# Optimization experiments

Hardware: AMD Instinct MI355X
Metric: run time of the kernel (lower is better)

The kernel has to match this reference:

```python
import jax, jax.numpy as jnp
import numpy as np

N, E, G = 200000, 800000, 8000
NODE_IN, EDGE_IN, H = 256, 64, 256


def _mlp2(h, w1, b1, w2, b2):
    return jax.nn.relu(h @ w1 + b1) @ w2 + b2


def setup_inputs() -> dict:
    key = jax.random.key(0)
    ks = jax.random.split(key, 30)
    s = 0.05
    p = lambda k, shp: (jax.random.normal(k, shp, jnp.float32) * s)
    inp = {
        "x": jax.random.normal(ks[0], (N, NODE_IN), jnp.float32),
        "edge_attr": jax.random.normal(ks[1], (E, EDGE_IN), jnp.float32),
        "edge_index": jax.random.randint(ks[2], (2, E), 0, N, dtype=jnp.int32),
        "batch": jnp.sort(jax.random.randint(ks[3], (N,), 0, G, dtype=jnp.int32)),
        # edge MLP
        "em_w1": p(ks[4], (EDGE_IN, H)), "em_b1": jnp.zeros((H,), jnp.float32),
        "em_w2": p(ks[5], (H, H)), "em_b2": jnp.zeros((H,), jnp.float32),
        # GINEConv 1 MLP
        "c1_w1": p(ks[6], (NODE_IN, H)), "c1_b1": jnp.zeros((H,), jnp.float32),
        "c1_w2": p(ks[7], (H, H)), "c1_b2": jnp.zeros((H,), jnp.float32),
        # GINEConv 2 MLP
        "c2_w1": p(ks[8], (H, H)), "c2_b1": jnp.zeros((H,), jnp.float32),
        "c2_w2": p(ks[9], (H, H)), "c2_b2": jnp.zeros((H,), jnp.float32),
        # heads
        "l1_w": p(ks[10], (H, 128)), "l1_b": jnp.zeros((128,), jnp.float32),
        "l2_w": p(ks[11], (128, 64)), "l2_b": jnp.zeros((64,), jnp.float32),
        "hS_w": p(ks[12], (64, 1)), "hS_b": jnp.zeros((1,), jnp.float32),
        "hP_w": p(ks[13], (64, 1)), "hP_b": jnp.zeros((1,), jnp.float32),
        "hN_w": p(ks[14], (64, 1)), "hN_b": jnp.zeros((1,), jnp.float32),
    }
    return inp


def _gine(x, ea, src, dst, w1, b1, w2, b2):
    # GINEConv (eps=0): out = MLP(x_i + sum_j relu(x_j + e_ji))
    msg = jax.nn.relu(x[src] + ea)                      # [E, H]
    agg = jax.ops.segment_sum(msg, dst, num_segments=x.shape[0])
    return _mlp2(x + agg, w1, b1, w2, b2)


def reference(x, edge_attr, edge_index, batch,
              em_w1, em_b1, em_w2, em_b2,
              c1_w1, c1_b1, c1_w2, c1_b2,
              c2_w1, c2_b1, c2_w2, c2_b2,
              l1_w, l1_b, l2_w, l2_b,
              hS_w, hS_b, hP_w, hP_b, hN_w, hN_b):
    src, dst = edge_index[0], edge_index[1]  # source_to_target flow
    ea = _mlp2(edge_attr, em_w1, em_b1, em_w2, em_b2)   # [E, 256]
    h = jax.nn.relu(_gine(x, ea, src, dst, c1_w1, c1_b1, c1_w2, c1_b2))
    h = jax.nn.relu(_gine(h, ea, src, dst, c2_w1, c2_b1, c2_w2, c2_b2))
    # global mean pool over graphs (dropout is identity in eval mode)
    sums = jax.ops.segment_sum(h, batch, num_segments=G)              # [G, 256]
    cnts = jax.ops.segment_sum(jnp.ones((h.shape[0],), h.dtype), batch, num_segments=G)
    pooled = sums / jnp.maximum(cnts, 1.0)[:, None]
    g = jax.nn.relu(pooled @ l1_w + l1_b)
    g = jax.nn.relu(g @ l2_w + l2_b)
    return ((g @ hS_w + hS_b).squeeze(-1),
            (g @ hP_w + hP_b).squeeze(-1),
            (g @ hN_w + hN_b).squeeze(-1))
```

## Files before the change

### kernel.cpp

```cpp
#include <hip/hip_runtime.h>
#include <hip/hip_bf16.h>

typedef __attribute__((ext_vector_type(8))) short short8;
typedef __attribute__((ext_vector_type(4))) float f32x4;
typedef __attribute__((ext_vector_type(2))) unsigned int u32x2;
typedef __attribute__((ext_vector_type(4))) unsigned int u32x4;

#define N_NODES  200000
#define N_EDGES  800000
#define N_GRAPHS 8000

__device__ __forceinline__ unsigned short f2bf(float f) {
  unsigned int u = __float_as_uint(f);
  unsigned int r = (u + 0x7fffu + ((u >> 16) & 1u)) >> 16;
  return (unsigned short)r;
}
__device__ __forceinline__ float bf2f(unsigned short s) {
  return __uint_as_float(((unsigned int)s) << 16);
}
__device__ __forceinline__ unsigned cvtpk(float a, float b) {
  union { __hip_bfloat162 h; unsigned u; } cv;
  cv.h = __float22bfloat162_rn(make_float2(a, b));
  return cv.u;
}

__device__ __forceinline__ void xpose4(unsigned W0, unsigned W1, int bsub,
                                       unsigned selT, unsigned& T0, unsigned& T1) {
  unsigned t0 = (unsigned)__shfl_xor((int)W0, 2);
  unsigned t1 = (unsigned)__shfl_xor((int)W1, 2);
  unsigned A0 = (bsub & 2) ? t1 : W0;
  unsigned A1 = (bsub & 2) ? W1 : t0;
  unsigned t2 = (unsigned)__shfl_xor((int)A0, 1);
  unsigned t3 = (unsigned)__shfl_xor((int)A1, 1);
  T0 = __builtin_amdgcn_perm(A0, t2, selT);
  T1 = __builtin_amdgcn_perm(A1, t3, selT);
}

__global__ void wtrans(const float* __restrict__ w, unsigned short* __restrict__ wt,
                       int K, int Nc) {
  int id = blockIdx.x * 256 + threadIdx.x;
  if (id >= K * Nc) return;
  int k = id / Nc, n = id % Nc;
  wt[n * K + k] = f2bf(w[id]);
}

__global__ __launch_bounds__(256) void f2bf_bulk(const float* __restrict__ x,
                                                 unsigned short* __restrict__ xb,
                                                 int n8) {
  int id = blockIdx.x * 256 + threadIdx.x;
  if (id >= n8) return;
  float4 a = ((const float4*)x)[id * 2];
  float4 b = ((const float4*)x)[id * 2 + 1];
  u32x4 pk = {cvtpk(a.x, a.y), cvtpk(a.z, a.w), cvtpk(b.x, b.y), cvtpk(b.z, b.w)};
  ((u32x4*)xb)[id] = pk;
}

template <int K1, int IN_MODE, int SLAB, int NKK>
__device__ __forceinline__ void stage_slab(
    int s, char* ab, int row0, int srow, int skk,
    const unsigned short* __restrict__ Xb,
    const unsigned short* __restrict__ aggb) {
#pragma unroll
  for (int c2 = 0; c2 < NKK; ++c2) {
    const int kloc = skk + 32 * c2;
    const int gk = s * SLAB + kloc;
    int off = srow * (2 * SLAB) + kloc * 2;
    off ^= (srow & 7) << 4;
    if (IN_MODE == 3) {
      u32x4 d = *(const u32x4*)(Xb + (size_t)(row0 + srow) * K1 + gk);
      *(u32x4*)(ab + off) = d;
    } else {
      const unsigned short* hp = Xb + (size_t)(row0 + srow) * 256 + gk;
      short8 hv = *(const short8*)hp;
      const unsigned short* ap = aggb + (size_t)(row0 + srow) * 256 + gk;
      short8 av = *(const short8*)ap;
      float v[8];
#pragma unroll
      for (int i = 0; i < 8; ++i)
        v[i] = bf2f((unsigned short)hv[i]) + bf2f((unsigned short)av[i]);
      u32x4 pk;
#pragma unroll
      for (int i = 0; i < 4; ++i) pk[i] = cvtpk(v[2 * i], v[2 * i + 1]);
      *(u32x4*)(ab + off) = pk;
    }
  }
}

template <int K1, int IN_MODE>
__global__ __launch_bounds__(256) void fused_mlp2(
    const unsigned short* __restrict__ Xb,
    const unsigned short* __restrict__ aggb,
    const unsigned short* __restrict__ w1t, const float* __restrict__ b1,
    const unsigned short* __restrict__ w2t, const float* __restrict__ b2,
    unsigned short* __restrict__ out, const int* __restrict__ perm,
    int relu_out) {
  constexpr int SLAB  = (K1 < 128) ? K1 : 128;
  constexpr int NSLAB = K1 / SLAB;
  constexpr int NKK   = SLAB / 32;
  __shared__ unsigned short h_lds[64 * 256];
  char* hbase = (char*)h_lds;

  const int tid  = threadIdx.x;
  const int row0 = blockIdx.x * 64;
  const int lane = tid & 63;
  const int wid  = tid >> 6;
  const int lr   = lane & 15;
  const int kq   = lane >> 4;
  const int col0 = wid * 64;
  const int bsub = lr & 3;
  const int asub = lr >> 2;
  const unsigned selT = (bsub & 1) ? 0x07060302u : 0x01000504u;

  const int srow = tid >> 2;
  const int skk  = (tid & 3) * 8;

  f32x4 acc[4][4];
#pragma unroll
  for (int m = 0; m < 4; ++m)
#pragma unroll
    for (int n = 0; n < 4; ++n) acc[m][n] = (f32x4){0.f, 0.f, 0.f, 0.f};

  float bias1[4];
#pragma unroll
  for (int n = 0; n < 4; ++n) bias1[n] = b1[col0 + n * 16 + lr];

  stage_slab<K1, IN_MODE, SLAB, NKK>(0, hbase, row0, srow, skk, Xb, aggb);
  __syncthreads();

#pragma unroll
  for (int s = 0; s < NSLAB; ++s) {
    if (s + 1 < NSLAB)
      stage_slab<K1, IN_MODE, SLAB, NKK>(s + 1, hbase + 16384, row0, srow, skk,
                                         Xb, aggb);
    char* ab = hbase + (s & 1) * 16384;
#pragma unroll
    for (int kk = 0; kk < NKK; ++kk) {
      short8 af[4], bq[4];
#pragma unroll
      for (int m = 0; m < 4; ++m) {
        int r = m * 16 + lr;
        int off = r * (2 * SLAB) + kk * 64 + kq * 16;
        off ^= (r & 7) << 4;
        af[m] = *(short8*)(ab + off);
      }
#pragma unroll
      for (int n = 0; n < 4; ++n) {
        int c = col0 + n * 16 + lr;
        bq[n] = *(const short8*)(w1t + (size_t)c * K1 + s * SLAB + kk * 32 + kq * 8);
      }
#pragma unroll
      for (int m = 0; m < 4; ++m)
#pragma unroll
        for (int n = 0; n < 4; ++n)
          acc[m][n] = __builtin_amdgcn_mfma_f32_16x16x32_bf16(af[m], bq[n], acc[m][n], 0, 0, 0);
    }
    __syncthreads();
  }

#pragma unroll
  for (int n = 0; n < 4; ++n) {
    float bn = bias1[n];
#pragma unroll
    for (int m = 0; m < 4; ++m) {
      float v0 = fmaxf(acc[m][n][0] + bn, 0.f);
      float v1 = fmaxf(acc[m][n][1] + bn, 0.f);
      float v2 = fmaxf(acc[m][n][2] + bn, 0.f);
      float v3 = fmaxf(acc[m][n][3] + bn, 0.f);
      unsigned W0 = cvtpk(v0, v1), W1 = cvtpk(v2, v3), T0, T1;
      xpose4(W0, W1, bsub, selT, T0, T1);
      int r = m * 16 + kq * 4 + bsub;
      int cb = col0 + n * 16 + asub * 4;
      int off = r * 512 + cb * 2;
      off ^= (r & 7) << 4;
      *(u32x2*)(hbase + off) = (u32x2){T0, T1};
    }
  }
  __syncthreads();

#pragma unroll
  for (int m = 0; m < 4; ++m)
#pragma unroll
    for (int n = 0; n < 4; ++n) acc[m][n] = (f32x4){0.f, 0.f, 0.f, 0.f};

  float bias2[4];
#pragma unroll
  for (int n = 0; n < 4; ++n) bias2[n] = b2[col0 + n * 16 + lr];

#pragma unroll
  for (int ks = 0; ks < 8; ++ks) {
    short8 af[4], bq[4];
#pragma unroll
    for (int m = 0; m < 4; ++m) {
      int r = m * 16 + lr;
      int off = r * 512 + ks * 64 + kq * 16;
      off ^= (r & 7) << 4;
      af[m] = *(short8*)(hbase + off);
    }
#pragma unroll
    for (int n = 0; n < 4; ++n) {
      int c = col0 + n * 16 + lr;
      bq[n] = *(const short8*)(w2t + (size_t)c * 256 + ks * 32 + kq * 8);
    }
#pragma unroll
    for (int m = 0; m < 4; ++m)
#pragma unroll
      for (int n = 0; n < 4; ++n)
        acc[m][n] = __builtin_amdgcn_mfma_f32_16x16x32_bf16(af[m], bq[n], acc[m][n], 0, 0, 0);
  }
  __syncthreads();

#pragma unroll
  for (int n = 0; n < 4; ++n) {
    float bn = bias2[n];
#pragma unroll
    for (int m = 0; m < 4; ++m) {
      float v0 = acc[m][n][0] + bn;
      float v1 = acc[m][n][1] + bn;
      float v2 = acc[m][n][2] + bn;
      float v3 = acc[m][n][3] + bn;
      if (relu_out) {
        v0 = fmaxf(v0, 0.f); v1 = fmaxf(v1, 0.f);
        v2 = fmaxf(v2, 0.f); v3 = fmaxf(v3, 0.f);
      }
      unsigned W0 = cvtpk(v0, v1), W1 = cvtpk(v2, v3), T0, T1;
      xpose4(W0, W1, bsub, selT, T0, T1);
      int r = m * 16 + kq * 4 + bsub;
      int cb = col0 + n * 16 + asub * 4;
      int off = r * 512 + cb * 2;
      off ^= (r & 7) << 4;
      *(u32x2*)(hbase + off) = (u32x2){T0, T1};
    }
  }
  __syncthreads();

#pragma unroll
  for (int it = 0; it < 8; ++it) {
    int r = (tid >> 5) + it * 8;
    int byte = (tid & 31) * 16;
    int off = (r * 512 + byte) ^ ((r & 7) << 4);
    u32x4 d = *(u32x4*)(hbase + off);
    int orow = perm ? perm[row0 + r] : (row0 + r);
    *(u32x4*)((char*)out + (size_t)orow * 512 + byte) = d;
  }
}

__global__ void hist_deg(const int* __restrict__ dst, int* __restrict__ rp) {
  int e = blockIdx.x * 256 + threadIdx.x;
  if (e < N_EDGES) atomicAdd(&rp[dst[e]], 1);
}

__global__ __launch_bounds__(256) void scan_block(int* __restrict__ rp,
                                                  int* __restrict__ bsum) {
  __shared__ int ts[256];
  int b = blockIdx.x, t = threadIdx.x;
  int base = b * 2048 + t * 8;
  int v[8]; int s = 0;
#pragma unroll
  for (int i = 0; i < 8; ++i) {
    int idx = base + i;
    v[i] = (idx < N_NODES) ? rp[idx] : 0;
    s += v[i];
  }
  ts[t] = s;
  __syncthreads();
#pragma unroll
  for (int off = 1; off < 256; off <<= 1) {
    int add = (t >= off) ? ts[t - off] : 0;
    __syncthreads();
    ts[t] += add;
    __syncthreads();
  }
  int excl = ts[t] - s;
  if (t == 255) bsum[b] = ts[255];
  int run = excl;
#pragma unroll
  for (int i = 0; i < 8; ++i) {
    int idx = base + i;
    if (idx < N_NODES) rp[idx] = run;
    run += v[i];
  }
}

__global__ __launch_bounds__(256) void scan_bsum(int* __restrict__ bsum, int nb) {
  __shared__ int ts[256];
  int t = threadIdx.x;
  int v = (t < nb) ? bsum[t] : 0;
  ts[t] = v;
  __syncthreads();
#pragma unroll
  for (int off = 1; off < 256; off <<= 1) {
    int add = (t >= off) ? ts[t - off] : 0;
    __syncthreads();
    ts[t] += add;
    __syncthreads();
  }
  if (t < nb) bsum[t] = ts[t] - v;
}

__global__ void scan_add(int* __restrict__ rp, const int* __restrict__ bsum) {
  int i = blockIdx.x * 256 + threadIdx.x;
  if (i < N_NODES) rp[i] += bsum[i >> 11];
}

__global__ void csr_fill(const int* __restrict__ src, const int* __restrict__ dst,
                         int* __restrict__ rp, int* __restrict__ csrc,
                         int* __restrict__ perm) {
  int e = blockIdx.x * 256 + threadIdx.x;
  if (e >= N_EDGES) return;
  int p = atomicAdd(&rp[dst[e]], 1);
  csrc[p] = src[e];
  perm[e] = p;
}

__global__ __launch_bounds__(256) void gather_agg(
    const unsigned short* __restrict__ ea, const unsigned short* __restrict__ xb,
    const int* __restrict__ rp, const int* __restrict__ csrc,
    unsigned short* __restrict__ agg) {
  int v = blockIdx.x * 4 + (threadIdx.x >> 6);
  if (v >= N_NODES) return;
  int lane = threadIdx.x & 63;
  int c = lane * 4;
  int beg = (v == 0) ? 0 : rp[v - 1];
  int end = rp[v];
  float a0 = 0.f, a1 = 0.f, a2 = 0.f, a3 = 0.f;
  int i = beg;
  for (; i + 2 <= end; i += 2) {
    int s0 = csrc[i];
    int s1 = csrc[i + 1];
    ushort4 e0 = *(const ushort4*)(ea + (size_t)i * 256 + c);
    ushort4 e1 = *(const ushort4*)(ea + (size_t)(i + 1) * 256 + c);
    ushort4 h0 = *(const ushort4*)(xb + (size_t)s0 * 256 + c);
    ushort4 h1 = *(const ushort4*)(xb + (size_t)s1 * 256 + c);
    a0 += fmaxf(bf2f(h0.x) + bf2f(e0.x), 0.f) + fmaxf(bf2f(h1.x) + bf2f(e1.x), 0.f);
    a1 += fmaxf(bf2f(h0.y) + bf2f(e0.y), 0.f) + fmaxf(bf2f(h1.y) + bf2f(e1.y), 0.f);
    a2 += fmaxf(bf2f(h0.z) + bf2f(e0.z), 0.f) + fmaxf(bf2f(h1.z) + bf2f(e1.z), 0.f);
    a3 += fmaxf(bf2f(h0.w) + bf2f(e0.w), 0.f) + fmaxf(bf2f(h1.w) + bf2f(e1.w), 0.f);
  }
  if (i < end) {
    int s0 = csrc[i];
    ushort4 ev = *(const ushort4*)(ea + (size_t)i * 256 + c);
    ushort4 hv = *(const ushort4*)(xb + (size_t)s0 * 256 + c);
    a0 += fmaxf(bf2f(hv.x) + bf2f(ev.x), 0.f);
    a1 += fmaxf(bf2f(hv.y) + bf2f(ev.y), 0.f);
    a2 += fmaxf(bf2f(hv.z) + bf2f(ev.z), 0.f);
    a3 += fmaxf(bf2f(hv.w) + bf2f(ev.w), 0.f);
  }
  u32x2 pk = {cvtpk(a0, a1), cvtpk(a2, a3)};
  *(u32x2*)(agg + (size_t)v * 256 + c) = pk;
}

__global__ __launch_bounds__(256) void pool_mean(const unsigned short* __restrict__ h2,
                                                 const int* __restrict__ batch,
                                                 float* __restrict__ pooled) {
  int g = blockIdx.x;
  int tid = threadIdx.x;
  int lane = tid & 63;
  int sub = tid >> 6;
  int lo = 0, hi = N_NODES;
  while (lo < hi) { int mid = (lo + hi) >> 1; if (batch[mid] < g) lo = mid + 1; else hi = mid; }
  int start = lo;
  hi = N_NODES;
  while (lo < hi) { int mid = (lo + hi) >> 1; if (batch[mid] < g + 1) lo = mid + 1; else hi = mid; }
  int end = lo;
  float s0 = 0.f, s1 = 0.f, s2 = 0.f, s3 = 0.f;
  for (int r = start + sub; r < end; r += 4) {
    ushort4 hv = *(const ushort4*)(h2 + (size_t)r * 256 + lane * 4);
    s0 += bf2f(hv.x); s1 += bf2f(hv.y); s2 += bf2f(hv.z); s3 += bf2f(hv.w);
  }
  __shared__ float4 red[4][64];
  red[sub][lane] = make_float4(s0, s1, s2, s3);
  __syncthreads();
  if (sub == 0) {
    float4 a = red[0][lane], b = red[1][lane], cc = red[2][lane], d = red[3][lane];
    float inv = 1.0f / fmaxf((float)(end - start), 1.0f);
    float4 t = make_float4((a.x + b.x + cc.x + d.x) * inv,
                           (a.y + b.y + cc.y + d.y) * inv,
                           (a.z + b.z + cc.z + d.z) * inv,
                           (a.w + b.w + cc.w + d.w) * inv);
    *(float4*)(pooled + (size_t)g * 256 + lane * 4) = t;
  }
}

__global__ __launch_bounds__(128) void head_mlp(
    const float* __restrict__ pooled, const float* __restrict__ l1w,
    const float* __restrict__ l1b, const float* __restrict__ l2w,
    const float* __restrict__ l2b, const float* __restrict__ hSw,
    const float* __restrict__ hSb, const float* __restrict__ hPw,
    const float* __restrict__ hPb, const float* __restrict__ hNw,
    const float* __restrict__ hNb, float* __restrict__ out) {
  int g = blockIdx.x, tid = threadIdx.x;
  __shared__ float p[256];
  __shared__ float g1[128];
  __shared__ float g2[64];
  p[tid] = pooled[(size_t)g * 256 + tid];
  p[tid + 128] = pooled[(size_t)g * 256 + tid + 128];
  __syncthreads();
  float a = l1b[tid];
#pragma unroll 8
  for (int k = 0; k < 256; ++k) a += p[k] * l1w[k * 128 + tid];
  g1[tid] = fmaxf(a, 0.f);
  __syncthreads();
  if (tid < 64) {
    float b = l2b[tid];
#pragma unroll 8
    for (int k = 0; k < 128; ++k) b += g1[k] * l2w[k * 64 + tid];
    g2[tid] = fmaxf(b, 0.f);
  }
  __syncthreads();
  if (tid < 64) {
    float v = g2[tid];
    float s = v * hSw[tid], pq = v * hPw[tid], nq = v * hNw[tid];
#pragma unroll
    for (int off = 32; off > 0; off >>= 1) {
      s  += __shfl_down(s, off);
      pq += __shfl_down(pq, off);
      nq += __shfl_down(nq, off);
    }
    if (tid == 0) {
      out[g]                = s  + hSb[0];
      out[N_GRAPHS + g]     = pq + hPb[0];
      out[2 * N_GRAPHS + g] = nq + hNb[0];
    }
  }
}

extern "C" void kernel_launch(void* const* d_in, const int* in_sizes, int n_in,
                              void* d_out, int out_size, void* d_ws, size_t ws_size,
                              hipStream_t stream) {
  const float* x         = (const float*)d_in[0];
  const float* edge_attr = (const float*)d_in[1];
  const int*   ei        = (const int*)d_in[2];
  const int*   batch     = (const int*)d_in[3];
  const float* em_w1 = (const float*)d_in[4];  const float* em_b1 = (const float*)d_in[5];
  const float* em_w2 = (const float*)d_in[6];  const float* em_b2 = (const float*)d_in[7];
  const float* c1_w1 = (const float*)d_in[8];  const float* c1_b1 = (const float*)d_in[9];
  const float* c1_w2 = (const float*)d_in[10]; const float* c1_b2 = (const float*)d_in[11];
  const float* c2_w1 = (const float*)d_in[12]; const float* c2_b1 = (const float*)d_in[13];
  const float* c2_w2 = (const float*)d_in[14]; const float* c2_b2 = (const float*)d_in[15];
  const float* l1_w = (const float*)d_in[16];  const float* l1_b = (const float*)d_in[17];
  const float* l2_w = (const float*)d_in[18];  const float* l2_b = (const float*)d_in[19];
  const float* hS_w = (const float*)d_in[20];  const float* hS_b = (const float*)d_in[21];
  const float* hP_w = (const float*)d_in[22];  const float* hP_b = (const float*)d_in[23];
  const float* hN_w = (const float*)d_in[24];  const float* hN_b = (const float*)d_in[25];

  char* ws = (char*)d_ws;
  unsigned short* ea     = (unsigned short*)ws;
  unsigned short* agg    = (unsigned short*)(ws + 409600000);
  unsigned short* xb     = (unsigned short*)(ws + 512000000);
  unsigned short* h1     = (unsigned short*)(ws + 614400000);
  unsigned short* eab    = h1;
  unsigned short* h2     = ea;
  float*          pooled = (float*)(ws + 716800000);
  int*            csrc   = (int*)(ws + 716800000);
  int*            perm   = (int*)(ws + 720000000);
  int*            rp     = (int*)(ws + 723200000);
  int*            bsum   = (int*)(ws + 724000000);
  unsigned short* wt     = (unsigned short*)(ws + 724992000);
  unsigned short* em_w1t = wt;
  unsigned short* em_w2t = em_w1t + 16384;
  unsigned short* c1_w1t = em_w2t + 65536;
  unsigned short* c1_w2t = c1_w1t + 65536;
  unsigned short* c2_w1t = c1_w2t + 65536;
  unsigned short* c2_w2t = c2_w1t + 65536;

  const int* srcI = ei;
  const int* dstI = ei + N_EDGES;

  wtrans<<<(16384 + 255) / 256, 256, 0, stream>>>(em_w1, em_w1t, 64, 256);
  wtrans<<<(65536 + 255) / 256, 256, 0, stream>>>(em_w2, em_w2t, 256, 256);
  wtrans<<<(65536 + 255) / 256, 256, 0, stream>>>(c1_w1, c1_w1t, 256, 256);
  wtrans<<<(65536 + 255) / 256, 256, 0, stream>>>(c1_w2, c1_w2t, 256, 256);
  wtrans<<<(65536 + 255) / 256, 256, 0, stream>>>(c2_w1, c2_w1t, 256, 256);
  wtrans<<<(65536 + 255) / 256, 256, 0, stream>>>(c2_w2, c2_w2t, 256, 256);

  f2bf_bulk<<<(N_NODES * 256 / 8 + 255) / 256, 256, 0, stream>>>(x, xb, N_NODES * 256 / 8);
  f2bf_bulk<<<(N_EDGES * 64 / 8 + 255) / 256, 256, 0, stream>>>(edge_attr, eab, N_EDGES * 64 / 8);

  hipMemsetAsync(rp, 0, (size_t)N_NODES * 4, stream);
  hist_deg<<<(N_EDGES + 255) / 256, 256, 0, stream>>>(dstI, rp);
  scan_block<<<(N_NODES + 2047) / 2048, 256, 0, stream>>>(rp, bsum);
  scan_bsum<<<1, 256, 0, stream>>>(bsum, (N_NODES + 2047) / 2048);
  scan_add<<<(N_NODES + 255) / 256, 256, 0, stream>>>(rp, bsum);
  csr_fill<<<N_EDGES / 256, 256, 0, stream>>>(srcI, dstI, rp, csrc, perm);

  fused_mlp2<64, 3><<<N_EDGES / 64, 256, 0, stream>>>(
      eab, nullptr, em_w1t, em_b1, em_w2t, em_b2, ea, perm, 0);

  gather_agg<<<(N_NODES + 3) / 4, 256, 0, stream>>>(ea, xb, rp, csrc, agg);
  fused_mlp2<256, 2><<<N_NODES / 64, 256, 0, stream>>>(
      xb, agg, c1_w1t, c1_b1, c1_w2t, c1_b2, h1, nullptr, 1);

  gather_agg<<<(N_NODES + 3) / 4, 256, 0, stream>>>(ea, h1, rp, csrc, agg);
  fused_mlp2<256, 2><<<N_NODES / 64, 256, 0, stream>>>(
      h1, agg, c2_w1t, c2_b1, c2_w2t, c2_b2, h2, nullptr, 1);

  pool_mean<<<N_GRAPHS, 256, 0, stream>>>(h2, batch, pooled);
  head_mlp<<<N_GRAPHS, 128, 0, stream>>>(pooled, l1_w, l1_b, l2_w, l2_b,
                                         hS_w, hS_b, hP_w, hP_b, hN_w, hN_b,
                                         (float*)d_out);
}
```

Before: 1.226 ms.

## Fuse neighbor gather-aggregation into GINE MLP slab staging

```diff
diff --git a/kernel.cpp b/kernel.cpp
--- a/kernel.cpp
+++ b/kernel.cpp
@@ -59,7 +59,8 @@
 __device__ __forceinline__ void stage_slab(
     int s, char* ab, int row0, int srow, int skk,
     const unsigned short* __restrict__ Xb,
-    const unsigned short* __restrict__ aggb) {
+    const unsigned short* __restrict__ ea,
+    const int* __restrict__ rp, const int* __restrict__ csrc) {
 #pragma unroll
   for (int c2 = 0; c2 < NKK; ++c2) {
     const int kloc = skk + 32 * c2;
@@ -70,17 +71,24 @@
       u32x4 d = *(const u32x4*)(Xb + (size_t)(row0 + srow) * K1 + gk);
       *(u32x4*)(ab + off) = d;
     } else {
-      const unsigned short* hp = Xb + (size_t)(row0 + srow) * 256 + gk;
-      short8 hv = *(const short8*)hp;
-      const unsigned short* ap = aggb + (size_t)(row0 + srow) * 256 + gk;
-      short8 av = *(const short8*)ap;
-      float v[8];
-#pragma unroll
-      for (int i = 0; i < 8; ++i)
-        v[i] = bf2f((unsigned short)hv[i]) + bf2f((unsigned short)av[i]);
+      const int v = row0 + srow;
+      const int beg = (v == 0) ? 0 : rp[v - 1];
+      const int end = rp[v];
+      short8 sv = *(const short8*)(Xb + (size_t)v * 256 + gk);
+      float acc8[8];
+#pragma unroll
+      for (int i = 0; i < 8; ++i) acc8[i] = bf2f((unsigned short)sv[i]);
+      for (int e = beg; e < end; ++e) {
+        int s0 = csrc[e];
+        short8 ev = *(const short8*)(ea + (size_t)e * 256 + gk);
+        short8 hv = *(const short8*)(Xb + (size_t)s0 * 256 + gk);
+#pragma unroll
+        for (int i = 0; i < 8; ++i)
+          acc8[i] += fmaxf(bf2f((unsigned short)hv[i]) + bf2f((unsigned short)ev[i]), 0.f);
+      }
       u32x4 pk;
 #pragma unroll
-      for (int i = 0; i < 4; ++i) pk[i] = cvtpk(v[2 * i], v[2 * i + 1]);
+      for (int i = 0; i < 4; ++i) pk[i] = cvtpk(acc8[2 * i], acc8[2 * i + 1]);
       *(u32x4*)(ab + off) = pk;
     }
   }
@@ -89,7 +97,8 @@
 template <int K1, int IN_MODE>
 __global__ __launch_bounds__(256) void fused_mlp2(
     const unsigned short* __restrict__ Xb,
-    const unsigned short* __restrict__ aggb,
+    const unsigned short* __restrict__ ea_csr,
+    const int* __restrict__ rp, const int* __restrict__ csrc,
     const unsigned short* __restrict__ w1t, const float* __restrict__ b1,
     const unsigned short* __restrict__ w2t, const float* __restrict__ b2,
     unsigned short* __restrict__ out, const int* __restrict__ perm,
@@ -124,14 +133,14 @@
 #pragma unroll
   for (int n = 0; n < 4; ++n) bias1[n] = b1[col0 + n * 16 + lr];
 
-  stage_slab<K1, IN_MODE, SLAB, NKK>(0, hbase, row0, srow, skk, Xb, aggb);
+  stage_slab<K1, IN_MODE, SLAB, NKK>(0, hbase, row0, srow, skk, Xb, ea_csr, rp, csrc);
   __syncthreads();
 
 #pragma unroll
   for (int s = 0; s < NSLAB; ++s) {
     if (s + 1 < NSLAB)
       stage_slab<K1, IN_MODE, SLAB, NKK>(s + 1, hbase + 16384, row0, srow, skk,
-                                         Xb, aggb);
+                                         Xb, ea_csr, rp, csrc);
     char* ab = hbase + (s & 1) * 16384;
 #pragma unroll
     for (int kk = 0; kk < NKK; ++kk) {
@@ -310,43 +319,6 @@
   int p = atomicAdd(&rp[dst[e]], 1);
   csrc[p] = src[e];
   perm[e] = p;
-}
-
-__global__ __launch_bounds__(256) void gather_agg(
-    const unsigned short* __restrict__ ea, const unsigned short* __restrict__ xb,
-    const int* __restrict__ rp, const int* __restrict__ csrc,
-    unsigned short* __restrict__ agg) {
-  int v = blockIdx.x * 4 + (threadIdx.x >> 6);
-  if (v >= N_NODES) return;
-  int lane = threadIdx.x & 63;
-  int c = lane * 4;
-  int beg = (v == 0) ? 0 : rp[v - 1];
-  int end = rp[v];
-  float a0 = 0.f, a1 = 0.f, a2 = 0.f, a3 = 0.f;
-  int i = beg;
-  for (; i + 2 <= end; i += 2) {
-    int s0 = csrc[i];
-    int s1 = csrc[i + 1];
-    ushort4 e0 = *(const ushort4*)(ea + (size_t)i * 256 + c);
-    ushort4 e1 = *(const ushort4*)(ea + (size_t)(i + 1) * 256 + c);
-    ushort4 h0 = *(const ushort4*)(xb + (size_t)s0 * 256 + c);
-    ushort4 h1 = *(const ushort4*)(xb + (size_t)s1 * 256 + c);
-    a0 += fmaxf(bf2f(h0.x) + bf2f(e0.x), 0.f) + fmaxf(bf2f(h1.x) + bf2f(e1.x), 0.f);
-    a1 += fmaxf(bf2f(h0.y) + bf2f(e0.y), 0.f) + fmaxf(bf2f(h1.y) + bf2f(e1.y), 0.f);
-    a2 += fmaxf(bf2f(h0.z) + bf2f(e0.z), 0.f) + fmaxf(bf2f(h1.z) + bf2f(e1.z), 0.f);
-    a3 += fmaxf(bf2f(h0.w) + bf2f(e0.w), 0.f) + fmaxf(bf2f(h1.w) + bf2f(e1.w), 0.f);
-  }
-  if (i < end) {
-    int s0 = csrc[i];
-    ushort4 ev = *(const ushort4*)(ea + (size_t)i * 256 + c);
-    ushort4 hv = *(const ushort4*)(xb + (size_t)s0 * 256 + c);
-    a0 += fmaxf(bf2f(hv.x) + bf2f(ev.x), 0.f);
-    a1 += fmaxf(bf2f(hv.y) + bf2f(ev.y), 0.f);
-    a2 += fmaxf(bf2f(hv.z) + bf2f(ev.z), 0.f);
-    a3 += fmaxf(bf2f(hv.w) + bf2f(ev.w), 0.f);
-  }
-  u32x2 pk = {cvtpk(a0, a1), cvtpk(a2, a3)};
-  *(u32x2*)(agg + (size_t)v * 256 + c) = pk;
 }
 
 __global__ __launch_bounds__(256) void pool_mean(const unsigned short* __restrict__ h2,
@@ -445,11 +417,10 @@
 
   char* ws = (char*)d_ws;
   unsigned short* ea     = (unsigned short*)ws;
-  unsigned short* agg    = (unsigned short*)(ws + 409600000);
+  unsigned short* h2     = (unsigned short*)(ws + 409600000);
   unsigned short* xb     = (unsigned short*)(ws + 512000000);
   unsigned short* h1     = (unsigned short*)(ws + 614400000);
   unsigned short* eab    = h1;
-  unsigned short* h2     = ea;
   float*          pooled = (float*)(ws + 716800000);
   int*            csrc   = (int*)(ws + 716800000);
   int*            perm   = (int*)(ws + 720000000);
@@ -484,15 +455,13 @@
   csr_fill<<<N_EDGES / 256, 256, 0, stream>>>(srcI, dstI, rp, csrc, perm);
 
   fused_mlp2<64, 3><<<N_EDGES / 64, 256, 0, stream>>>(
-      eab, nullptr, em_w1t, em_b1, em_w2t, em_b2, ea, perm, 0);
-
-  gather_agg<<<(N_NODES + 3) / 4, 256, 0, stream>>>(ea, xb, rp, csrc, agg);
-  fused_mlp2<256, 2><<<N_NODES / 64, 256, 0, stream>>>(
-      xb, agg, c1_w1t, c1_b1, c1_w2t, c1_b2, h1, nullptr, 1);
-
-  gather_agg<<<(N_NODES + 3) / 4, 256, 0, stream>>>(ea, h1, rp, csrc, agg);
-  fused_mlp2<256, 2><<<N_NODES / 64, 256, 0, stream>>>(
-      h1, agg, c2_w1t, c2_b1, c2_w2t, c2_b2, h2, nullptr, 1);
+      eab, nullptr, nullptr, nullptr, em_w1t, em_b1, em_w2t, em_b2, ea, perm, 0);
+
+  fused_mlp2<256, 4><<<N_NODES / 64, 256, 0, stream>>>(
+      xb, ea, rp, csrc, c1_w1t, c1_b1, c1_w2t, c1_b2, h1, nullptr, 1);
+
+  fused_mlp2<256, 4><<<N_NODES / 64, 256, 0, stream>>>(
+      h1, ea, rp, csrc, c2_w1t, c2_b1, c2_w2t, c2_b2, h2, nullptr, 1);
 
   pool_mean<<<N_GRAPHS, 256, 0, stream>>>(h2, batch, pooled);
   head_mlp<<<N_GRAPHS, 128, 0, stream>>>(pooled, l1_w, l1_b, l2_w, l2_b,
```

New measurement: 1.708 ms. 1.39x slower.
